# Performance work log

Hardware: AMD Instinct MI355X
Metric: run time of the kernel (lower is better)

## Reference

```python
import jax, jax.numpy as jnp
import numpy as np

N, P, K, DIMS = 32, 1024, 16, 3
C_IN, C_MID, C_OUT, DM = 64, 64, 128, 2


def setup_inputs() -> dict:
    key = jax.random.key(0)
    ks = jax.random.split(key, 12)
    s = 0.05
    return {
        "rep_pt": jax.random.normal(ks[0], (N, P, DIMS), jnp.float32),
        "pts": jax.random.normal(ks[1], (N, P, K, DIMS), jnp.float32),
        "fts": jax.random.normal(ks[2], (N, P, K, C_IN), jnp.float32),
        # dense1 / dense2 (Linear + ELU)
        "w1": jax.random.normal(ks[3], (DIMS, C_MID), jnp.float32) * s,
        "b1": jnp.zeros((C_MID,), jnp.float32),
        "w2": jax.random.normal(ks[4], (C_MID, C_MID), jnp.float32) * s,
        "b2": jnp.zeros((C_MID,), jnp.float32),
        # conv2d: Conv2d(dims, K*K, (1,K)) -> weight (K*K, dims, K) (kernel h=1 squeezed)
        "wconv": jax.random.normal(ks[5], (K * K, DIMS, K), jnp.float32) * s,
        "bconv": jnp.zeros((K * K,), jnp.float32),
        # depthwise Conv2d(K, K*K, (1,K), groups=K) -> weight (K,K,K) [group i, mult j, tap k]
        "wdep1": jax.random.normal(ks[6], (K, K, K), jnp.float32) * s,
        "bdep1": jnp.zeros((K, K), jnp.float32),
        "wdep2": jax.random.normal(ks[7], (K, K, K), jnp.float32) * s,
        "bdep2": jnp.zeros((K, K), jnp.float32),
        # SepConv: depthwise Conv2d(C, C*DM, (1,K), groups=C) + pointwise Conv2d(C*DM, C_out, 1)
        "wdw": jax.random.normal(ks[8], (C_MID + C_IN, DM, K), jnp.float32) * s,
        "bdw": jnp.zeros((C_MID + C_IN, DM), jnp.float32),
        "wpw": jax.random.normal(ks[9], (C_OUT, C_MID + C_IN, DM), jnp.float32) * s,
        "bpw": jnp.zeros((C_OUT,), jnp.float32),
    }


def reference(rep_pt, pts, fts, w1, b1, w2, b2, wconv, bconv,
              wdep1, bdep1, wdep2, bdep2, wdw, bdw, wpw, bpw):
    n, p, k, _ = pts.shape
    # localize neighbors around representative point
    pts_local = pts - rep_pt[:, :, None, :]                      # (N,P,K,dims)
    # lift point coords to C_mid features (two Linear+ELU)
    h = jax.nn.elu(pts_local @ w1 + b1)
    h = jax.nn.elu(h @ w2 + b2)                                  # (N,P,K,C_mid)
    fts_cat = jnp.concatenate([h, fts], axis=-1)                 # (N,P,K,C_mid+C_in)
    # Conv2d(dims -> K*K, kernel (1,K)): full contraction over neighbor axis k
    X = jax.nn.elu(jnp.einsum('npkc,ock->npo', pts_local, wconv) + bconv)
    X = X.reshape(n, p, k, k)                                    # (N,P,K,K)
    # depthwise convs, groups=K, depth_multiplier=K, kernel (1,K):
    # channels-last input channel is last K axis (i), conv taps run over third axis (k)
    X = jax.nn.elu(jnp.einsum('npki,ijk->npij', X, wdep1) + bdep1)
    X = jnp.einsum('npki,ijk->npij', X, wdep2) + bdep2           # (N,P,K,K), no activation
    # learned X-transform applied to features
    fts_X = jnp.einsum('npkj,npjc->npkc', X, fts_cat)            # (N,P,K,C_mid+C_in)
    # separable conv over neighbor axis: depthwise (1,K) then pointwise 1x1
    tmp = jnp.einsum('npkc,cmk->npcm', fts_X, wdw) + bdw         # (N,P,C,DM)
    out = jax.nn.elu(jnp.einsum('npcm,ocm->npo', tmp, wpw) + bpw)
    return out                                                   # (N,P,C_out)
```

## Files before the change

kernel.cpp:

```cpp
#include <hip/hip_runtime.h>
#include <hip/hip_bf16.h>


#define ELU(x) ((x) > 0.0f ? (x) : (__expf(x) - 1.0f))

__device__ __forceinline__ void lds_fence() {
    asm volatile("s_waitcnt lgkmcnt(0)" ::: "memory");
}

typedef __attribute__((ext_vector_type(8))) short short8v;
typedef __attribute__((ext_vector_type(4))) float f32x4;
typedef __attribute__((ext_vector_type(2))) unsigned int uint2v;
#define MFMA32(a, b, c) __builtin_amdgcn_mfma_f32_16x16x32_bf16(a, b, c, 0, 0, 0)

__device__ __forceinline__ short f2bf(float x) {
    __hip_bfloat16 h = __float2bfloat16(x);
    return *reinterpret_cast<short*>(&h);
}
__device__ __forceinline__ float bf2f(short x) {
    unsigned u = ((unsigned)(unsigned short)x) << 16;
    return __uint_as_float(u);
}
__device__ __forceinline__ unsigned packbf(float a, float b) {
    return (unsigned)(unsigned short)f2bf(a) | (((unsigned)(unsigned short)f2bf(b)) << 16);
}
__device__ __forceinline__ void gload_lds16(const float* g, float* l) {
    __builtin_amdgcn_global_load_lds(
        (const __attribute__((address_space(1))) void*)g,
        (__attribute__((address_space(3))) void*)l,
        16, 0, 0);
}
__device__ __forceinline__ float xor32_add(float q) {
    uint2v r = __builtin_amdgcn_permlane32_swap(__float_as_uint(q), __float_as_uint(q), false, false);
    return __uint_as_float(r.x) + __uint_as_float(r.y);
}

#define XW_WC   0
#define XW_WD1  8192
#define XW_WD2  12352
#define XW_BC   16512
#define XW_BD1  16768
#define XW_BD2  17024
#define XW_SCR  17280
#define XW_TOTAL (17280 + 4*4368)

__global__ __launch_bounds__(256) void k_xform(
    const float* __restrict__ rep, const float* __restrict__ pts,
    const float* __restrict__ wconv, const float* __restrict__ bconv,
    const float* __restrict__ wdep1, const float* __restrict__ bdep1,
    const float* __restrict__ wdep2, const float* __restrict__ bdep2,
    unsigned short* __restrict__ x2bf)
{
    extern __shared__ __align__(16) float sm[];
    short* smh = (short*)sm;
    const int tid = threadIdx.x;

    for (int e = tid; e < 2048; e += 256) {
        const int part = e >> 10, u = (e >> 6) & 15, l = e & 63;
        const int g = l >> 4, s = l & 15;
        const int o = u * 16 + s;
        short8v v;
        if (part == 0) {
            #pragma unroll
            for (int t = 0; t < 8; ++t) v[t] = f2bf(wconv[o*48 + g*8 + t]);
        } else {
            #pragma unroll
            for (int t = 0; t < 4; ++t) v[t] = f2bf(wconv[o*48 + 32 + g*4 + t]);
            #pragma unroll
            for (int t = 4; t < 8; ++t) v[t] = 0;
        }
        *(short8v*)&smh[e * 8] = v;
    }
    for (int e = tid; e < 4096; e += 256) {
        const int i = e >> 8, j = (e >> 4) & 15, k = e & 15;
        sm[XW_WD1 + i*260 + j*16 + k] = wdep1[e];
        sm[XW_WD2 + i*260 + j*16 + k] = wdep2[e];
    }
    sm[XW_BC  + tid] = bconv[tid];
    sm[XW_BD1 + tid] = bdep1[tid];
    sm[XW_BD2 + tid] = bdep2[tid];
    __syncthreads();

    const int wave = tid >> 6, lane = tid & 63;
    const int g = lane >> 4, s = lane & 15;
    const int pt0 = (blockIdx.x * 4 + wave) * 16;

    const int p = pt0 + s;
    const float r0 = rep[p*3], r1 = rep[p*3+1], r2 = rep[p*3+2];
    short8v ah0, al0, ah1, al1;
    #pragma unroll
    for (int e = 0; e < 8; ++e) {
        const int r = g*8 + e;
        const int d = g >> 1, k = r & 15;
        const float v = pts[p*48 + k*3 + d] - (d == 0 ? r0 : r1);
        const short h = f2bf(v);
        ah0[e] = h; al0[e] = f2bf(v - bf2f(h));
    }
    #pragma unroll
    for (int e = 0; e < 4; ++e) {
        const int k = g*4 + e;
        const float v = pts[p*48 + k*3 + 2] - r2;
        const short h = f2bf(v);
        ah1[e] = h; al1[e] = f2bf(v - bf2f(h));
    }
    #pragma unroll
    for (int e = 4; e < 8; ++e) { ah1[e] = 0; al1[e] = 0; }

    f32x4 ex[16];
    #pragma unroll
    for (int u = 0; u < 16; ++u) {
        const float b = sm[XW_BC + u*16 + s];
        f32x4 acc; acc[0] = b; acc[1] = b; acc[2] = b; acc[3] = b;
        const short8v bh0 = *(const short8v*)&smh[(u*64 + lane) * 8];
        const short8v bh1 = *(const short8v*)&smh[((16 + u)*64 + lane) * 8];
        acc = MFMA32(ah0, bh0, acc);
        acc = MFMA32(ah1, bh1, acc);
        acc = MFMA32(al0, bh0, acc);
        acc = MFMA32(al1, bh1, acc);
        f32x4 r;
        r[0] = ELU(acc[0]); r[1] = ELU(acc[1]); r[2] = ELU(acc[2]); r[3] = ELU(acc[3]);
        ex[u] = r;
    }

    const int scrb = XW_SCR + wave * 4368;
    #pragma unroll
    for (int j = 0; j < 16; ++j) {
        const float b = sm[XW_BD1 + s*16 + j];
        f32x4 a; a[0] = b; a[1] = b; a[2] = b; a[3] = b;
        #pragma unroll
        for (int kb = 0; kb < 4; ++kb) {
            const float4 w = *(const float4*)&sm[XW_WD1 + s*260 + j*16 + kb*4];
            a += ex[kb*4+0] * w.x; a += ex[kb*4+1] * w.y;
            a += ex[kb*4+2] * w.z; a += ex[kb*4+3] * w.w;
        }
        #pragma unroll
        for (int q = 0; q < 4; ++q)
            sm[scrb + (g*4+q)*273 + j*17 + s] = ELU(a[q]);
    }
    lds_fence();

    f32x4 xr[16];
    #pragma unroll
    for (int k = 0; k < 16; ++k) {
        f32x4 v;
        #pragma unroll
        for (int q = 0; q < 4; ++q)
            v[q] = sm[scrb + (g*4+q)*273 + s*17 + k];
        xr[k] = v;
    }
    f32x4 oj[16];
    #pragma unroll
    for (int j = 0; j < 16; ++j) {
        const float b = sm[XW_BD2 + s*16 + j];
        f32x4 a; a[0] = b; a[1] = b; a[2] = b; a[3] = b;
        #pragma unroll
        for (int kb = 0; kb < 4; ++kb) {
            const float4 w = *(const float4*)&sm[XW_WD2 + s*260 + j*16 + kb*4];
            a += xr[kb*4+0] * w.x; a += xr[kb*4+1] * w.y;
            a += xr[kb*4+2] * w.z; a += xr[kb*4+3] * w.w;
        }
        oj[j] = a;
    }
    #pragma unroll
    for (int q = 0; q < 4; ++q) {
        const int pp = pt0 + g*4 + q;
        #pragma unroll
        for (int jb = 0; jb < 4; ++jb) {
            uint2 pk;
            pk.x = packbf(oj[jb*4+0][q], oj[jb*4+1][q]);
            pk.y = packbf(oj[jb*4+2][q], oj[jb*4+3][q]);
            *(uint2*)&x2bf[(size_t)pp*256 + s*16 + jb*4] = pk;
        }
    }
}

#define NPTS 32768
#define TOTW 3072
__global__ __launch_bounds__(256, 3) void k_feat(
    const float* __restrict__ rep, const float* __restrict__ pts, const float* __restrict__ fts,
    const float* __restrict__ w1, const float* __restrict__ b1,
    const float* __restrict__ w2, const float* __restrict__ b2,
    const float* __restrict__ wdw, const float* __restrict__ bdw,
    const unsigned short* __restrict__ x2bf, unsigned short* __restrict__ tmpbf)
{
    __shared__ __align__(16) short sw2[4096];
    __shared__ __align__(16) uint2 sw1[64];
    __shared__ float sbdw[256];
    __shared__ __align__(16) float sfts[4][2][1024];
    const int tid = threadIdx.x;

    for (int idx = tid; idx < 512; idx += 256) {
        const int r = idx >> 6, l = idx & 63;
        const int nt = r >> 1, h = r & 1, gg = l >> 4, ss = l & 15;
        short8v v;
        #pragma unroll
        for (int e = 0; e < 8; ++e)
            v[e] = f2bf(w2[(h*32 + gg*8 + e)*64 + nt*16 + ss]);
        *(short8v*)&sw2[idx * 8] = v;
    }
    if (tid < 64) {
        const int j = tid;
        uint2 v;
        v.x = packbf(w1[j], w1[64 + j]);
        v.y = packbf(w1[128 + j], b1[j]);
        sw1[j] = v;
    }
    sbdw[tid] = bdw[tid];
    __syncthreads();

    const int lane = tid & 63, wave = tid >> 6;
    const int g = lane >> 4, s = lane & 15;

    float b2c[4];
    #pragma unroll
    for (int nt = 0; nt < 4; ++nt) b2c[nt] = b2[nt*16 + s];

    uint2 wp0[8], wp1[8];
    #pragma unroll
    for (int u = 0; u < 8; ++u) {
        const int cb = (u*16 + s) * 32 + 4*g;
        wp0[u].x = packbf(wdw[cb + 0],  wdw[cb + 1]);
        wp0[u].y = packbf(wdw[cb + 2],  wdw[cb + 3]);
        wp1[u].x = packbf(wdw[cb + 16], wdw[cb + 17]);
        wp1[u].y = packbf(wdw[cb + 18], wdw[cb + 19]);
    }

    const int gw = blockIdx.x * 4 + wave;
    float* sf0 = &sfts[wave][0][0];
    float* sf1 = &sfts[wave][1][0];

    {
        const float* src = fts + (size_t)gw * 1024 + lane * 4;
        #pragma unroll
        for (int i = 0; i < 4; ++i) gload_lds16(src + i*256, sf0 + i*256);
    }
    ushort4 xv_n = *(const ushort4*)&x2bf[(size_t)gw*256 + s*16 + g*4];
    float p0_n = pts[gw*48 + s*3 + 0] - rep[gw*3 + 0];
    float p1_n = pts[gw*48 + s*3 + 1] - rep[gw*3 + 1];
    float p2_n = pts[gw*48 + s*3 + 2] - rep[gw*3 + 2];

    int k = 0;
    for (int pt = gw; pt < NPTS; pt += TOTW, ++k) {
        float* sfc = (k & 1) ? sf1 : sf0;
        float* sfn = (k & 1) ? sf0 : sf1;
        const int ptn = pt + TOTW;

        if (ptn < NPTS) {
            const float* src = fts + (size_t)ptn * 1024 + lane * 4;
            #pragma unroll
            for (int i = 0; i < 4; ++i) gload_lds16(src + i*256, sfn + i*256);
        }
        asm volatile("s_waitcnt vmcnt(4)" ::: "memory");

        const ushort4 xv = xv_n;
        const float p0 = p0_n, p1 = p1_n, p2 = p2_n;

        if (ptn < NPTS) {
            xv_n = *(const ushort4*)&x2bf[(size_t)ptn*256 + s*16 + g*4];
            p0_n = pts[ptn*48 + s*3 + 0] - rep[ptn*3 + 0];
            p1_n = pts[ptn*48 + s*3 + 1] - rep[ptn*3 + 1];
            p2_n = pts[ptn*48 + s*3 + 2] - rep[ptn*3 + 2];
        }

        short8v af0, af1;
        #pragma unroll
        for (int t = 0; t < 2; ++t) {
            short8v f;
            #pragma unroll
            for (int e = 0; e < 8; ++e) {
                const uint2 pk = sw1[t*32 + g*8 + e];
                const float wx = __uint_as_float(pk.x << 16);
                const float wy = __uint_as_float(pk.x & 0xffff0000u);
                const float wz = __uint_as_float(pk.y << 16);
                const float bb = __uint_as_float(pk.y & 0xffff0000u);
                float h = bb + p0*wx + p1*wy + p2*wz;
                h = ELU(h);
                f[e] = f2bf(h);
            }
            if (t == 0) af0 = f; else af1 = f;
        }
        f32x4 hacc[4];
        #pragma unroll
        for (int nt = 0; nt < 4; ++nt) {
            f32x4 a; a[0] = b2c[nt]; a[1] = b2c[nt]; a[2] = b2c[nt]; a[3] = b2c[nt];
            const short8v bf0 = *(const short8v*)&sw2[((nt*2 + 0)*64 + lane) * 8];
            const short8v bf1 = *(const short8v*)&sw2[((nt*2 + 1)*64 + lane) * 8];
            a = MFMA32(af0, bf0, a);
            a = MFMA32(af1, bf1, a);
            hacc[nt] = a;
        }
        short8v a2 = (short8v)0;
        a2[0] = (short)xv.x; a2[1] = (short)xv.y;
        a2[2] = (short)xv.z; a2[3] = (short)xv.w;

        float q0a[8], q1a[8];
        #pragma unroll
        for (int u = 0; u < 8; ++u) {
            short8v bfrag = (short8v)0;
            if (u < 4) {
                #pragma unroll
                for (int q = 0; q < 4; ++q) bfrag[q] = f2bf(ELU(hacc[u][q]));
            } else {
                #pragma unroll
                for (int e = 0; e < 4; ++e)
                    bfrag[e] = f2bf(sfc[(g*4 + e)*64 + (u - 4)*16 + s]);
            }
            f32x4 z; z[0] = 0.f; z[1] = 0.f; z[2] = 0.f; z[3] = 0.f;
            const f32x4 fx = MFMA32(a2, bfrag, z);

            const float a0 = __uint_as_float(wp0[u].x << 16);
            const float a1 = __uint_as_float(wp0[u].x & 0xffff0000u);
            const float a2f = __uint_as_float(wp0[u].y << 16);
            const float a3 = __uint_as_float(wp0[u].y & 0xffff0000u);
            const float c0 = __uint_as_float(wp1[u].x << 16);
            const float c1 = __uint_as_float(wp1[u].x & 0xffff0000u);
            const float c2 = __uint_as_float(wp1[u].y << 16);
            const float c3 = __uint_as_float(wp1[u].y & 0xffff0000u);
            q0a[u] = fx[0]*a0 + fx[1]*a1 + fx[2]*a2f + fx[3]*a3;
            q1a[u] = fx[0]*c0 + fx[1]*c1 + fx[2]*c2 + fx[3]*c3;
        }
        #pragma unroll
        for (int u = 0; u < 8; ++u) {
            q0a[u] += __shfl_xor(q0a[u], 16);
            q1a[u] += __shfl_xor(q1a[u], 16);
        }
        #pragma unroll
        for (int u = 0; u < 8; ++u) {
            q0a[u] = xor32_add(q0a[u]);
            q1a[u] = xor32_add(q1a[u]);
        }
        if (lane < 16) {
            #pragma unroll
            for (int u = 0; u < 8; ++u) {
                const int c = u*16 + s;
                const unsigned pk = packbf(q0a[u] + sbdw[2*c], q1a[u] + sbdw[2*c + 1]);
                *(unsigned*)&tmpbf[(size_t)pt*256 + 2*c] = pk;
            }
        }
    }
}

__global__ __launch_bounds__(256) void k_out(
    const unsigned short* __restrict__ tmp, const float* __restrict__ wpw,
    const float* __restrict__ bpw, float* __restrict__ out)
{
    __shared__ unsigned sb[16384];
    const int tid = threadIdx.x;
    for (int e = tid; e < 16384; e += 256) {
        const int n = e >> 7, kw = e & 127;
        const int cb = kw >> 2, wi = kw & 3;
        const unsigned lo = (unsigned)(unsigned short)f2bf(wpw[n*256 + 2*kw]);
        const unsigned hi = (unsigned)(unsigned short)f2bf(wpw[n*256 + 2*kw + 1]);
        sb[n*128 + ((cb ^ (n & 7)) << 2) + wi] = lo | (hi << 16);
    }
    __syncthreads();

    const int lane = tid & 63, wave = tid >> 6;
    const int g = lane >> 4, s = lane & 15;
    const int row = blockIdx.x * 64 + wave * 16 + s;

    f32x4 acc[8];
    #pragma unroll
    for (int nt = 0; nt < 8; ++nt) {
        const float b = bpw[nt*16 + s];
        acc[nt][0] = b; acc[nt][1] = b; acc[nt][2] = b; acc[nt][3] = b;
    }

    const unsigned short* arow = tmp + (size_t)row * 256 + g*8;
    short8v pa = *(const short8v*)(arow);

    #pragma unroll
    for (int kk = 0; kk < 8; ++kk) {
        const short8v a = pa;
        if (kk < 7) pa = *(const short8v*)(arow + (kk+1)*32);
        #pragma unroll
        for (int nt = 0; nt < 8; ++nt) {
            const short8v bf = *(const short8v*)&sb[(nt*16 + s)*128 + (((kk*4 + g) ^ (s & 7)) << 2)];
            acc[nt] = MFMA32(a, bf, acc[nt]);
        }
    }
    const int rbase = blockIdx.x * 64 + wave * 16 + 4*g;
    #pragma unroll
    for (int nt = 0; nt < 8; ++nt)
        #pragma unroll
        for (int q = 0; q < 4; ++q)
            out[(size_t)(rbase + q) * 128 + nt*16 + s] = ELU(acc[nt][q]);
}

extern "C" void kernel_launch(void* const* d_in, const int* in_sizes, int n_in,
                              void* d_out, int out_size, void* d_ws, size_t ws_size,
                              hipStream_t stream)
{
    (void)in_sizes; (void)n_in; (void)out_size; (void)ws_size;
    const float* rep   = (const float*)d_in[0];
    const float* pts   = (const float*)d_in[1];
    const float* fts   = (const float*)d_in[2];
    const float* w1    = (const float*)d_in[3];
    const float* b1    = (const float*)d_in[4];
    const float* w2    = (const float*)d_in[5];
    const float* b2    = (const float*)d_in[6];
    const float* wconv = (const float*)d_in[7];
    const float* bconv = (const float*)d_in[8];
    const float* wdep1 = (const float*)d_in[9];
    const float* bdep1 = (const float*)d_in[10];
    const float* wdep2 = (const float*)d_in[11];
    const float* bdep2 = (const float*)d_in[12];
    const float* wdw   = (const float*)d_in[13];
    const float* bdw   = (const float*)d_in[14];
    const float* wpw   = (const float*)d_in[15];
    const float* bpw   = (const float*)d_in[16];
    float* out  = (float*)d_out;
    unsigned short* x2bf  = (unsigned short*)d_ws;
    unsigned short* tmpbf = (unsigned short*)((char*)d_ws + (size_t)32 * 1024 * 1024);

    hipFuncSetAttribute((const void*)k_xform, hipFuncAttributeMaxDynamicSharedMemorySize, XW_TOTAL*4);

    k_xform<<<dim3(512), dim3(256), XW_TOTAL*4, stream>>>(rep, pts, wconv, bconv, wdep1, bdep1, wdep2, bdep2, x2bf);
    k_feat <<<dim3(768), dim3(256), 0, stream>>>(rep, pts, fts, w1, b1, w2, b2, wdw, bdw, x2bf, tmpbf);
    k_out  <<<dim3(512), dim3(256), 0, stream>>>(tmpbf, wpw, bpw, out);
}
```

Baseline: 93.90 us.

## Process two points per wave iteration in k_feat with swizzled LDS feature buffer

Each wave in k_feat now handles a pair of points per loop iteration instead of one. The two points run interleaved, independent MFMA and ELU chains, which should raise instruction-level parallelism and amortise the weight LDS reads. The fts staging buffer doubles to hold two points, and an XOR swizzle on the LDS layout is added to cut bank conflicts. The grid shrinks from 768 to 512 blocks. The cost is higher register and LDS pressure, which may reduce occupancy, and a deeper vmcnt wait.

Result: slower. 97.38 us (+3.7%).

```diff
diff --git a/kernel.cpp b/kernel.cpp
--- a/kernel.cpp
+++ b/kernel.cpp
@@ -174,8 +174,8 @@
     }
 }
 
-#define NPTS 32768
-#define TOTW 3072
+#define NPAIRS 16384
+#define TOTWP 2048
 __global__ __launch_bounds__(256, 3) void k_feat(
     const float* __restrict__ rep, const float* __restrict__ pts, const float* __restrict__ fts,
     const float* __restrict__ w1, const float* __restrict__ b1,
@@ -186,7 +186,7 @@
     __shared__ __align__(16) short sw2[4096];
     __shared__ __align__(16) uint2 sw1[64];
     __shared__ float sbdw[256];
-    __shared__ __align__(16) float sfts[4][2][1024];
+    __shared__ __align__(16) float sfts[4][2][2048];
     const int tid = threadIdx.x;
 
     for (int idx = tid; idx < 512; idx += 256) {
@@ -210,6 +210,7 @@
 
     const int lane = tid & 63, wave = tid >> 6;
     const int g = lane >> 4, s = lane & 15;
+    const int g8 = g * 8;
 
     float b2c[4];
     #pragma unroll
@@ -225,88 +226,117 @@
         wp1[u].y = packbf(wdw[cb + 18], wdw[cb + 19]);
     }
 
-    const int gw = blockIdx.x * 4 + wave;
+    const int pw = blockIdx.x * 4 + wave;
     float* sf0 = &sfts[wave][0][0];
     float* sf1 = &sfts[wave][1][0];
 
     {
-        const float* src = fts + (size_t)gw * 1024 + lane * 4;
-        #pragma unroll
-        for (int i = 0; i < 4; ++i) gload_lds16(src + i*256, sf0 + i*256);
-    }
-    ushort4 xv_n = *(const ushort4*)&x2bf[(size_t)gw*256 + s*16 + g*4];
-    float p0_n = pts[gw*48 + s*3 + 0] - rep[gw*3 + 0];
-    float p1_n = pts[gw*48 + s*3 + 1] - rep[gw*3 + 1];
-    float p2_n = pts[gw*48 + s*3 + 2] - rep[gw*3 + 2];
+        const float* base = fts + (size_t)(2*pw) * 1024;
+        #pragma unroll
+        for (int a = 0; a < 2; ++a)
+            #pragma unroll
+            for (int i = 0; i < 4; ++i)
+                gload_lds16(base + a*1024 + i*256 + (lane ^ (2*i))*4, sf0 + a*1024 + i*256);
+    }
+    ushort4 xvn0, xvn1; float pn0[3], pn1[3];
+    {
+        const int pt0i = 2*pw, pt1i = 2*pw + 1;
+        xvn0 = *(const ushort4*)&x2bf[(size_t)pt0i*256 + s*16 + g*4];
+        xvn1 = *(const ushort4*)&x2bf[(size_t)pt1i*256 + s*16 + g*4];
+        pn0[0] = pts[pt0i*48 + s*3 + 0] - rep[pt0i*3 + 0];
+        pn0[1] = pts[pt0i*48 + s*3 + 1] - rep[pt0i*3 + 1];
+        pn0[2] = pts[pt0i*48 + s*3 + 2] - rep[pt0i*3 + 2];
+        pn1[0] = pts[pt1i*48 + s*3 + 0] - rep[pt1i*3 + 0];
+        pn1[1] = pts[pt1i*48 + s*3 + 1] - rep[pt1i*3 + 1];
+        pn1[2] = pts[pt1i*48 + s*3 + 2] - rep[pt1i*3 + 2];
+    }
 
     int k = 0;
-    for (int pt = gw; pt < NPTS; pt += TOTW, ++k) {
+    for (int pr = pw; pr < NPAIRS; pr += TOTWP, ++k) {
         float* sfc = (k & 1) ? sf1 : sf0;
         float* sfn = (k & 1) ? sf0 : sf1;
-        const int ptn = pt + TOTW;
-
-        if (ptn < NPTS) {
-            const float* src = fts + (size_t)ptn * 1024 + lane * 4;
-            #pragma unroll
-            for (int i = 0; i < 4; ++i) gload_lds16(src + i*256, sfn + i*256);
-        }
-        asm volatile("s_waitcnt vmcnt(4)" ::: "memory");
-
-        const ushort4 xv = xv_n;
-        const float p0 = p0_n, p1 = p1_n, p2 = p2_n;
-
-        if (ptn < NPTS) {
-            xv_n = *(const ushort4*)&x2bf[(size_t)ptn*256 + s*16 + g*4];
-            p0_n = pts[ptn*48 + s*3 + 0] - rep[ptn*3 + 0];
-            p1_n = pts[ptn*48 + s*3 + 1] - rep[ptn*3 + 1];
-            p2_n = pts[ptn*48 + s*3 + 2] - rep[ptn*3 + 2];
-        }
-
-        short8v af0, af1;
-        #pragma unroll
-        for (int t = 0; t < 2; ++t) {
-            short8v f;
-            #pragma unroll
-            for (int e = 0; e < 8; ++e) {
-                const uint2 pk = sw1[t*32 + g*8 + e];
-                const float wx = __uint_as_float(pk.x << 16);
-                const float wy = __uint_as_float(pk.x & 0xffff0000u);
-                const float wz = __uint_as_float(pk.y << 16);
-                const float bb = __uint_as_float(pk.y & 0xffff0000u);
-                float h = bb + p0*wx + p1*wy + p2*wz;
-                h = ELU(h);
-                f[e] = f2bf(h);
+        const int prn = pr + TOTWP;
+
+        if (prn < NPAIRS) {
+            const float* base = fts + (size_t)(2*prn) * 1024;
+            #pragma unroll
+            for (int a = 0; a < 2; ++a)
+                #pragma unroll
+                for (int i = 0; i < 4; ++i)
+                    gload_lds16(base + a*1024 + i*256 + (lane ^ (2*i))*4, sfn + a*1024 + i*256);
+        }
+        asm volatile("s_waitcnt vmcnt(24)" ::: "memory");
+
+        const ushort4 xv0 = xvn0, xv1 = xvn1;
+        const float p00 = pn0[0], p01 = pn0[1], p02 = pn0[2];
+        const float p10 = pn1[0], p11 = pn1[1], p12 = pn1[2];
+
+        if (prn < NPAIRS) {
+            const int n0 = 2*prn, n1 = 2*prn + 1;
+            xvn0 = *(const ushort4*)&x2bf[(size_t)n0*256 + s*16 + g*4];
+            xvn1 = *(const ushort4*)&x2bf[(size_t)n1*256 + s*16 + g*4];
+            pn0[0] = pts[n0*48 + s*3 + 0] - rep[n0*3 + 0];
+            pn0[1] = pts[n0*48 + s*3 + 1] - rep[n0*3 + 1];
+            pn0[2] = pts[n0*48 + s*3 + 2] - rep[n0*3 + 2];
+            pn1[0] = pts[n1*48 + s*3 + 0] - rep[n1*3 + 0];
+            pn1[1] = pts[n1*48 + s*3 + 1] - rep[n1*3 + 1];
+            pn1[2] = pts[n1*48 + s*3 + 2] - rep[n1*3 + 2];
+        }
+
+        f32x4 hacc0[4], hacc1[4];
+        {
+            short8v af00, af01, af10, af11;
+            #pragma unroll
+            for (int t = 0; t < 2; ++t) {
+                short8v f0, f1;
+                #pragma unroll
+                for (int e = 0; e < 8; ++e) {
+                    const uint2 pk = sw1[t*32 + g*8 + e];
+                    const float wx = __uint_as_float(pk.x << 16);
+                    const float wy = __uint_as_float(pk.x & 0xffff0000u);
+                    const float wz = __uint_as_float(pk.y << 16);
+                    const float bb = __uint_as_float(pk.y & 0xffff0000u);
+                    float h0 = bb + p00*wx + p01*wy + p02*wz;
+                    float h1 = bb + p10*wx + p11*wy + p12*wz;
+                    h0 = ELU(h0); h1 = ELU(h1);
+                    f0[e] = f2bf(h0); f1[e] = f2bf(h1);
+                }
+                if (t == 0) { af00 = f0; af10 = f1; } else { af01 = f0; af11 = f1; }
             }
-            if (t == 0) af0 = f; else af1 = f;
-        }
-        f32x4 hacc[4];
-        #pragma unroll
-        for (int nt = 0; nt < 4; ++nt) {
-            f32x4 a; a[0] = b2c[nt]; a[1] = b2c[nt]; a[2] = b2c[nt]; a[3] = b2c[nt];
-            const short8v bf0 = *(const short8v*)&sw2[((nt*2 + 0)*64 + lane) * 8];
-            const short8v bf1 = *(const short8v*)&sw2[((nt*2 + 1)*64 + lane) * 8];
-            a = MFMA32(af0, bf0, a);
-            a = MFMA32(af1, bf1, a);
-            hacc[nt] = a;
-        }
-        short8v a2 = (short8v)0;
-        a2[0] = (short)xv.x; a2[1] = (short)xv.y;
-        a2[2] = (short)xv.z; a2[3] = (short)xv.w;
-
-        float q0a[8], q1a[8];
+            #pragma unroll
+            for (int nt = 0; nt < 4; ++nt) {
+                f32x4 a0, a1;
+                a0[0] = b2c[nt]; a0[1] = b2c[nt]; a0[2] = b2c[nt]; a0[3] = b2c[nt];
+                a1 = a0;
+                const short8v bf0 = *(const short8v*)&sw2[((nt*2 + 0)*64 + lane) * 8];
+                const short8v bf1 = *(const short8v*)&sw2[((nt*2 + 1)*64 + lane) * 8];
+                a0 = MFMA32(af00, bf0, a0); a0 = MFMA32(af01, bf1, a0);
+                a1 = MFMA32(af10, bf0, a1); a1 = MFMA32(af11, bf1, a1);
+                hacc0[nt] = a0; hacc1[nt] = a1;
+            }
+        }
+        short8v a20 = (short8v)0, a21 = (short8v)0;
+        a20[0] = (short)xv0.x; a20[1] = (short)xv0.y; a20[2] = (short)xv0.z; a20[3] = (short)xv0.w;
+        a21[0] = (short)xv1.x; a21[1] = (short)xv1.y; a21[2] = (short)xv1.z; a21[3] = (short)xv1.w;
+
+        f32x4 z; z[0] = 0.f; z[1] = 0.f; z[2] = 0.f; z[3] = 0.f;
+        float q00[8], q01[8], q10[8], q11[8];
         #pragma unroll
         for (int u = 0; u < 8; ++u) {
-            short8v bfrag = (short8v)0;
+            short8v bfr0 = (short8v)0, bfr1 = (short8v)0;
             if (u < 4) {
                 #pragma unroll
-                for (int q = 0; q < 4; ++q) bfrag[q] = f2bf(ELU(hacc[u][q]));
+                for (int q = 0; q < 4; ++q) { bfr0[q] = f2bf(ELU(hacc0[u][q])); bfr1[q] = f2bf(ELU(hacc1[u][q])); }
             } else {
                 #pragma unroll
-                for (int e = 0; e < 4; ++e)
-                    bfrag[e] = f2bf(sfc[(g*4 + e)*64 + (u - 4)*16 + s]);
+                for (int e = 0; e < 4; ++e) {
+                    const int off = (g*4 + e)*64 + ((((u - 4)*16 + s)) ^ g8);
+                    bfr0[e] = f2bf(sfc[off]);
+                    bfr1[e] = f2bf(sfc[1024 + off]);
+                }
             }
-            f32x4 z; z[0] = 0.f; z[1] = 0.f; z[2] = 0.f; z[3] = 0.f;
-            const f32x4 fx = MFMA32(a2, bfrag, z);
+            const f32x4 fx0 = MFMA32(a20, bfr0, z);
+            const f32x4 fx1 = MFMA32(a21, bfr1, z);
 
             const float a0 = __uint_as_float(wp0[u].x << 16);
             const float a1 = __uint_as_float(wp0[u].x & 0xffff0000u);
@@ -316,25 +346,32 @@
             const float c1 = __uint_as_float(wp1[u].x & 0xffff0000u);
             const float c2 = __uint_as_float(wp1[u].y << 16);
             const float c3 = __uint_as_float(wp1[u].y & 0xffff0000u);
-            q0a[u] = fx[0]*a0 + fx[1]*a1 + fx[2]*a2f + fx[3]*a3;
-            q1a[u] = fx[0]*c0 + fx[1]*c1 + fx[2]*c2 + fx[3]*c3;
+            q00[u] = fx0[0]*a0 + fx0[1]*a1 + fx0[2]*a2f + fx0[3]*a3;
+            q01[u] = fx0[0]*c0 + fx0[1]*c1 + fx0[2]*c2 + fx0[3]*c3;
+            q10[u] = fx1[0]*a0 + fx1[1]*a1 + fx1[2]*a2f + fx1[3]*a3;
+            q11[u] = fx1[0]*c0 + fx1[1]*c1 + fx1[2]*c2 + fx1[3]*c3;
         }
         #pragma unroll
         for (int u = 0; u < 8; ++u) {
-            q0a[u] += __shfl_xor(q0a[u], 16);
-            q1a[u] += __shfl_xor(q1a[u], 16);
+            q00[u] += __shfl_xor(q00[u], 16);
+            q01[u] += __shfl_xor(q01[u], 16);
+            q10[u] += __shfl_xor(q10[u], 16);
+            q11[u] += __shfl_xor(q11[u], 16);
         }
         #pragma unroll
         for (int u = 0; u < 8; ++u) {
-            q0a[u] = xor32_add(q0a[u]);
-            q1a[u] = xor32_add(q1a[u]);
+            q00[u] = xor32_add(q00[u]);
+            q01[u] = xor32_add(q01[u]);
+            q10[u] = xor32_add(q10[u]);
+            q11[u] = xor32_add(q11[u]);
         }
         if (lane < 16) {
+            const size_t b0 = (size_t)(2*pr) * 256, b1 = (size_t)(2*pr + 1) * 256;
             #pragma unroll
             for (int u = 0; u < 8; ++u) {
                 const int c = u*16 + s;
-                const unsigned pk = packbf(q0a[u] + sbdw[2*c], q1a[u] + sbdw[2*c + 1]);
-                *(unsigned*)&tmpbf[(size_t)pt*256 + 2*c] = pk;
+                *(unsigned*)&tmpbf[b0 + 2*c] = packbf(q00[u] + sbdw[2*c], q01[u] + sbdw[2*c + 1]);
+                *(unsigned*)&tmpbf[b1 + 2*c] = packbf(q10[u] + sbdw[2*c], q11[u] + sbdw[2*c + 1]);
             }
         }
     }
@@ -416,6 +453,6 @@
     hipFuncSetAttribute((const void*)k_xform, hipFuncAttributeMaxDynamicSharedMemorySize, XW_TOTAL*4);
 
     k_xform<<<dim3(512), dim3(256), XW_TOTAL*4, stream>>>(rep, pts, wconv, bconv, wdep1, bdep1, wdep2, bdep2, x2bf);
-    k_feat <<<dim3(768), dim3(256), 0, stream>>>(rep, pts, fts, w1, b1, w2, b2, wdw, bdw, x2bf, tmpbf);
+    k_feat <<<dim3(512), dim3(256), 0, stream>>>(rep, pts, fts, w1, b1, w2, b2, wdw, bdw, x2bf, tmpbf);
     k_out  <<<dim3(512), dim3(256), 0, stream>>>(tmpbf, wpw, bpw, out);
 }
```
